# Kernel tuning notes

Measured on AMD Instinct MI355X. Metric: run time of the kernel, lower is better.

The kernel has to match this reference:

```python
import jax, jax.numpy as jnp
import numpy as np

N, E, F_IN, G = 100000, 1600000, 128, 64
H1, H2, H3 = 64, 32, 16


def _xavier(key, fan_in, fan_out):
    lim = np.sqrt(6.0 / (fan_in + fan_out))
    return jax.random.uniform(key, (fan_in, fan_out), jnp.float32, -lim, lim)


def setup_inputs() -> dict:
    key = jax.random.key(0)
    ks = jax.random.split(key, 16)
    x = jax.random.normal(ks[0], (N, F_IN), jnp.float32)
    edge_index = jax.random.randint(ks[1], (2, E), 0, N, dtype=jnp.int32)
    batch = jnp.sort(jax.random.randint(ks[2], (N,), 0, G, dtype=jnp.int32))
    d = {
        "x": x,
        "W1": _xavier(ks[3], F_IN, H1), "b1": jnp.zeros((H1,), jnp.float32),
        "W2": _xavier(ks[4], H1, H2), "b2": jnp.zeros((H2,), jnp.float32),
        "W3": _xavier(ks[5], H2, H3), "b3": jnp.zeros((H3,), jnp.float32),
        "g1": jnp.ones((H1,), jnp.float32), "be1": jnp.zeros((H1,), jnp.float32),
        "g2": jnp.ones((H2,), jnp.float32), "be2": jnp.zeros((H2,), jnp.float32),
        "g3": jnp.ones((H3,), jnp.float32), "be3": jnp.zeros((H3,), jnp.float32),
        "attn_w": _xavier(ks[6], 3 * H3, 3), "attn_b": jnp.zeros((3,), jnp.float32),
        "fc1_w": _xavier(ks[7], H3, H3), "fc1_b": jnp.zeros((H3,), jnp.float32),
        "fc2_w": _xavier(ks[8], H3, H3 // 2), "fc2_b": jnp.zeros((H3 // 2,), jnp.float32),
        "out_w": _xavier(ks[9], H3 // 2, 1), "out_b": jnp.zeros((1,), jnp.float32),
        "edge_index": edge_index,
        "batch": batch,
        "num_graphs": G,
    }
    return d


def _lrelu(z):
    return jnp.where(z > 0, z, 0.1 * z)


def _bn(h, gamma, beta, eps=1e-5):
    # BatchNorm1d forward with batch statistics (biased variance), as torch training-mode math
    m = jnp.mean(h, axis=0)
    v = jnp.mean(jnp.square(h - m), axis=0)
    return (h - m) * jax.lax.rsqrt(v + eps) * gamma + beta


def reference(x, W1, b1, W2, b2, W3, b3, g1, be1, g2, be2, g3, be3,
              attn_w, attn_b, fc1_w, fc1_b, fc2_w, fc2_b, out_w, out_b,
              edge_index, batch, num_graphs):
    src, dst = edge_index[0], edge_index[1]
    n = x.shape[0]
    # GCN degree with self-loops: deg[i] = 1 + #incoming edges
    deg = jax.ops.segment_sum(jnp.ones((src.shape[0],), x.dtype), dst, num_segments=n) + 1.0
    dis = jax.lax.rsqrt(deg)                      # deg^-1/2, [N]
    enorm = dis[src] * dis[dst]                   # per-edge norm, [E]
    selfw = dis * dis                             # self-loop norm, [N]

    def gcn(h, W, b):
        hw = h @ W                                # [N, H]
        agg = jax.ops.segment_sum(hw[src] * enorm[:, None], dst, num_segments=n)
        return agg + selfw[:, None] * hw + b

    x1 = _lrelu(_bn(gcn(x, W1, b1), g1, be1))     # dropout = identity (eval)
    x2 = _lrelu(_bn(gcn(x1, W2, b2), g2, be2))    # residual skipped: 64 != 32
    x3 = _lrelu(_bn(gcn(x2, W3, b3), g3, be3))    # residual skipped: 32 != 16

    # multi-pool over graphs
    ones_n = jnp.ones((n,), x.dtype)
    counts = jax.ops.segment_sum(ones_n, batch, num_segments=num_graphs)  # [G]
    x_sum = jax.ops.segment_sum(x3, batch, num_segments=num_graphs)       # [G, H3]
    x_mean = x_sum / jnp.maximum(counts, 1.0)[:, None]
    x_max = jax.ops.segment_max(x3, batch, num_segments=num_graphs)

    pooled = jnp.concatenate([x_mean, x_max, x_sum], axis=1)              # [G, 3*H3]
    aw = jax.nn.softmax(pooled @ attn_w + attn_b, axis=1)                 # [G, 3]
    xg = aw[:, 0:1] * x_mean + aw[:, 1:2] * x_max + aw[:, 2:3] * x_sum    # [G, H3]

    xg = _lrelu(xg @ fc1_w + fc1_b)
    xg = _lrelu(xg @ fc2_w + fc2_b)
    out = jax.nn.sigmoid(xg @ out_w + out_b)                              # [G, 1]
    return out
```

## Files before the change

kernel.cpp:

```cpp
#include <hip/hip_runtime.h>

#define GG 64
typedef unsigned long long ull;
typedef unsigned short u16;

__device__ __forceinline__ u16 f2b(float x) {
    unsigned u = __float_as_uint(x);
    return (u16)((u + 0x7FFFu + ((u >> 16) & 1u)) >> 16);
}

__device__ __forceinline__ void add8(const uint4 q, float* acc) {
    acc[0] += __uint_as_float(q.x << 16);
    acc[1] += __uint_as_float(q.x & 0xFFFF0000u);
    acc[2] += __uint_as_float(q.y << 16);
    acc[3] += __uint_as_float(q.y & 0xFFFF0000u);
    acc[4] += __uint_as_float(q.z << 16);
    acc[5] += __uint_as_float(q.z & 0xFFFF0000u);
    acc[6] += __uint_as_float(q.w << 16);
    acc[7] += __uint_as_float(q.w & 0xFFFF0000u);
}

__global__ void k_hist(const int* __restrict__ dst, int* __restrict__ cnt, int E) {
    int e = blockIdx.x * blockDim.x + threadIdx.x;
    if (e < E) atomicAdd(&cnt[dst[e]], 1);
}

__global__ void k_dis(const int* __restrict__ cnt, float* __restrict__ dis, int n) {
    int i = blockIdx.x * blockDim.x + threadIdx.x;
    if (i < n) dis[i] = rsqrtf((float)cnt[i] + 1.0f);
}

__global__ void k_scanA(const int* __restrict__ cnt, int* __restrict__ rp,
                        int* __restrict__ bsum, int n) {
    __shared__ int s[256];
    int i = blockIdx.x * 256 + threadIdx.x;
    int v = (i < n) ? cnt[i] : 0;
    s[threadIdx.x] = v;
    __syncthreads();
    for (int off = 1; off < 256; off <<= 1) {
        int t = (threadIdx.x >= off) ? s[threadIdx.x - off] : 0;
        __syncthreads();
        s[threadIdx.x] += t;
        __syncthreads();
    }
    if (i < n) rp[i] = s[threadIdx.x] - v;
    if (threadIdx.x == 255) bsum[blockIdx.x] = s[255];
}

__global__ void k_scanB(int* __restrict__ bsum, int nb) {
    __shared__ int s[512];
    int v = (threadIdx.x < nb) ? bsum[threadIdx.x] : 0;
    s[threadIdx.x] = v;
    __syncthreads();
    for (int off = 1; off < 512; off <<= 1) {
        int t = (threadIdx.x >= off) ? s[threadIdx.x - off] : 0;
        __syncthreads();
        s[threadIdx.x] += t;
        __syncthreads();
    }
    if (threadIdx.x < nb) bsum[threadIdx.x] = s[threadIdx.x] - v;
}

__global__ void k_scanC(int* __restrict__ rp, const int* __restrict__ bsum,
                        int* __restrict__ cursor, int n, int E) {
    int i = blockIdx.x * 256 + threadIdx.x;
    if (i < n) {
        int r = rp[i] + bsum[blockIdx.x];
        rp[i] = r;
        cursor[i] = r;
    }
    if (i == 0) rp[n] = E;
}

__global__ __launch_bounds__(256) void k_scatter(const int* __restrict__ src,
                                                 const int* __restrict__ dst,
                                                 int* __restrict__ cursor,
                                                 ull* __restrict__ epack, int E, int n) {
    const int part = blockIdx.x & 7;
    const int nblk = gridDim.x >> 3;
    const int bser = blockIdx.x >> 3;
    const int lo = (int)(((long long)part * n) >> 3);
    const int hi = (part == 7) ? n : (int)(((long long)(part + 1) * n) >> 3);
    for (int e = bser * 256 + threadIdx.x; e < E; e += nblk * 256) {
        int d = dst[e];
        if (d >= lo && d < hi) {
            int s = src[e];
            int pos = atomicAdd(&cursor[d], 1);
            epack[pos] = (ull)(unsigned)s;
        }
    }
}

template <int FIN, int FOUT, bool BN>
__global__ __launch_bounds__(256) void k_mm(const float* __restrict__ h,
                                            const float* __restrict__ W,
                                            const float* __restrict__ dis,
                                            const float* __restrict__ stats,
                                            const float* __restrict__ gma,
                                            const float* __restrict__ bta,
                                            u16* __restrict__ hw, int n) {
    constexpr int FX  = FOUT / 4;
    constexpr int TY  = 256 / FX;
    constexpr int NT  = TY * 4;
    constexpr int LDA = FIN + ((FOUT == 64) ? 2 : 1);
    __shared__ float sA[NT * LDA];
    __shared__ float sW[FIN * FOUT];
    __shared__ float sSc[FIN], sSh[FIN];

    if (BN && threadIdx.x < FIN) {
        int f = threadIdx.x;
        float inv_n = 1.0f / (float)n;
        float m = stats[f] * inv_n;
        float var = fmaxf(stats[64 + f] * inv_n - m * m, 0.f);
        float sc = rsqrtf(var + 1e-5f) * gma[f];
        sSc[f] = sc;
        sSh[f] = bta[f] - m * sc;
    }
    for (int i = threadIdx.x; i < FIN * FOUT / 4; i += 256)
        ((float4*)sW)[i] = ((const float4*)W)[i];
    if (BN) __syncthreads();

    const int node0 = blockIdx.x * NT;
    constexpr int LD4 = NT * FIN / 4 / 256;
    #pragma unroll
    for (int i = 0; i < LD4; ++i) {
        int idx4 = i * 256 + threadIdx.x;
        int row = idx4 / (FIN / 4);
        int c4  = idx4 % (FIN / 4);
        int gn  = node0 + row;
        float4 v = make_float4(0.f, 0.f, 0.f, 0.f);
        if (gn < n) v = ((const float4*)(h + (long long)gn * FIN))[c4];
        if (BN) {
            int f = c4 * 4;
            float t;
            t = fmaf(v.x, sSc[f + 0], sSh[f + 0]); v.x = t > 0.f ? t : 0.1f * t;
            t = fmaf(v.y, sSc[f + 1], sSh[f + 1]); v.y = t > 0.f ? t : 0.1f * t;
            t = fmaf(v.z, sSc[f + 2], sSh[f + 2]); v.z = t > 0.f ? t : 0.1f * t;
            t = fmaf(v.w, sSc[f + 3], sSh[f + 3]); v.w = t > 0.f ? t : 0.1f * t;
        }
        float* p = &sA[row * LDA + c4 * 4];
        p[0] = v.x; p[1] = v.y; p[2] = v.z; p[3] = v.w;
    }
    __syncthreads();

    const int tx = threadIdx.x % FX;
    const int ty = threadIdx.x / FX;
    float acc[4][4];
    #pragma unroll
    for (int i = 0; i < 4; ++i)
        #pragma unroll
        for (int j = 0; j < 4; ++j) acc[i][j] = 0.f;

    #pragma unroll 8
    for (int k = 0; k < FIN; ++k) {
        float4 wv = *((const float4*)&sW[k * FOUT + tx * 4]);
        float a0 = sA[(ty * 4 + 0) * LDA + k];
        float a1 = sA[(ty * 4 + 1) * LDA + k];
        float a2 = sA[(ty * 4 + 2) * LDA + k];
        float a3 = sA[(ty * 4 + 3) * LDA + k];
        acc[0][0] = fmaf(a0, wv.x, acc[0][0]); acc[0][1] = fmaf(a0, wv.y, acc[0][1]);
        acc[0][2] = fmaf(a0, wv.z, acc[0][2]); acc[0][3] = fmaf(a0, wv.w, acc[0][3]);
        acc[1][0] = fmaf(a1, wv.x, acc[1][0]); acc[1][1] = fmaf(a1, wv.y, acc[1][1]);
        acc[1][2] = fmaf(a1, wv.z, acc[1][2]); acc[1][3] = fmaf(a1, wv.w, acc[1][3]);
        acc[2][0] = fmaf(a2, wv.x, acc[2][0]); acc[2][1] = fmaf(a2, wv.y, acc[2][1]);
        acc[2][2] = fmaf(a2, wv.z, acc[2][2]); acc[2][3] = fmaf(a2, wv.w, acc[2][3]);
        acc[3][0] = fmaf(a3, wv.x, acc[3][0]); acc[3][1] = fmaf(a3, wv.y, acc[3][1]);
        acc[3][2] = fmaf(a3, wv.z, acc[3][2]); acc[3][3] = fmaf(a3, wv.w, acc[3][3]);
    }

    #pragma unroll
    for (int i = 0; i < 4; ++i) {
        int gn = node0 + ty * 4 + i;
        if (gn < n) {
            float dv = dis[gn];
            ushort4 o;
            o.x = f2b(acc[i][0] * dv); o.y = f2b(acc[i][1] * dv);
            o.z = f2b(acc[i][2] * dv); o.w = f2b(acc[i][3] * dv);
            ((ushort4*)(hw + (long long)gn * FOUT))[tx] = o;
        }
    }
}

template <int FOUT>
__global__ __launch_bounds__(256) void k_agg(const u16* __restrict__ hwb,
                                             const ull* __restrict__ epack,
                                             const int* __restrict__ rp,
                                             const float* __restrict__ dis,
                                             const float* __restrict__ bias,
                                             float* __restrict__ y,
                                             float* __restrict__ stats, int n) {
    constexpr int LPN = FOUT / 8;
    constexpr int NPB = 256 / LPN;
    constexpr int RS  = FOUT / 8;
    __shared__ float ssum[FOUT], ssq[FOUT];
    for (int i = threadIdx.x; i < FOUT; i += 256) { ssum[i] = 0.f; ssq[i] = 0.f; }
    __syncthreads();
    const int local = threadIdx.x / LPN;
    const int fq = threadIdx.x % LPN;
    const uint4* hw4 = (const uint4*)hwb;
    float b8[8];
    #pragma unroll
    for (int i = 0; i < 8; ++i) b8[i] = bias[fq * 8 + i];
    float lsum[8] = {0,0,0,0,0,0,0,0}, lsq[8] = {0,0,0,0,0,0,0,0};

    int node = blockIdx.x * NPB + local;
    if (node < n) {
        int j0 = rp[node], j1 = rp[node + 1];
        float acc[8] = {0,0,0,0,0,0,0,0};
        int j = j0;
        for (; j + 8 <= j1; j += 8) {
            int s0 = (int)(unsigned)epack[j + 0];
            int s1 = (int)(unsigned)epack[j + 1];
            int s2 = (int)(unsigned)epack[j + 2];
            int s3 = (int)(unsigned)epack[j + 3];
            int s4 = (int)(unsigned)epack[j + 4];
            int s5 = (int)(unsigned)epack[j + 5];
            int s6 = (int)(unsigned)epack[j + 6];
            int s7 = (int)(unsigned)epack[j + 7];
            uint4 q0 = hw4[(long long)s0 * RS + fq];
            uint4 q1 = hw4[(long long)s1 * RS + fq];
            uint4 q2 = hw4[(long long)s2 * RS + fq];
            uint4 q3 = hw4[(long long)s3 * RS + fq];
            uint4 q4 = hw4[(long long)s4 * RS + fq];
            uint4 q5 = hw4[(long long)s5 * RS + fq];
            uint4 q6 = hw4[(long long)s6 * RS + fq];
            uint4 q7 = hw4[(long long)s7 * RS + fq];
            add8(q0, acc); add8(q1, acc); add8(q2, acc); add8(q3, acc);
            add8(q4, acc); add8(q5, acc); add8(q6, acc); add8(q7, acc);
        }
        for (; j + 2 <= j1; j += 2) {
            int s0 = (int)(unsigned)epack[j + 0];
            int s1 = (int)(unsigned)epack[j + 1];
            uint4 q0 = hw4[(long long)s0 * RS + fq];
            uint4 q1 = hw4[(long long)s1 * RS + fq];
            add8(q0, acc); add8(q1, acc);
        }
        for (; j < j1; ++j) {
            uint4 q = hw4[(long long)(unsigned)epack[j] * RS + fq];
            add8(q, acc);
        }
        uint4 qs = hw4[(long long)node * RS + fq];
        add8(qs, acc);
        float dv = dis[node];
        #pragma unroll
        for (int i = 0; i < 8; ++i) acc[i] = fmaf(dv, acc[i], b8[i]);
        float4* y4 = (float4*)y;
        long long o = (long long)node * (FOUT / 4) + fq * 2;
        y4[o]     = make_float4(acc[0], acc[1], acc[2], acc[3]);
        y4[o + 1] = make_float4(acc[4], acc[5], acc[6], acc[7]);
        #pragma unroll
        for (int i = 0; i < 8; ++i) {
            lsum[i] += acc[i];
            lsq[i] = fmaf(acc[i], acc[i], lsq[i]);
        }
    }
    #pragma unroll
    for (int i = 0; i < 8; ++i) {
        atomicAdd(&ssum[fq * 8 + i], lsum[i]);
        atomicAdd(&ssq[fq * 8 + i], lsq[i]);
    }
    __syncthreads();
    for (int i = threadIdx.x; i < FOUT; i += 256) {
        atomicAdd(&stats[i], ssum[i]);
        atomicAdd(&stats[64 + i], ssq[i]);
    }
}

__global__ void k_pool_graph(const float* __restrict__ yraw, const int* __restrict__ batch,
                             const float* __restrict__ stats, const float* __restrict__ gma,
                             const float* __restrict__ bta, int n,
                             float* __restrict__ psum, float* __restrict__ pmax,
                             float* __restrict__ pcnt) {
    const int g = blockIdx.x;
    const int f = threadIdx.x & 15;
    float inv_n = 1.0f / (float)n;
    float m = stats[f] * inv_n;
    float var = fmaxf(stats[64 + f] * inv_n - m * m, 0.f);
    float sc = rsqrtf(var + 1e-5f) * gma[f];
    float sh = bta[f] - m * sc;

    __shared__ int s_lo, s_hi;
    if (threadIdx.x == 0) {
        int lo = 0, hi = n;
        while (lo < hi) { int mid = (lo + hi) >> 1; if (batch[mid] < g) lo = mid + 1; else hi = mid; }
        s_lo = lo;
        hi = n;
        while (lo < hi) { int mid = (lo + hi) >> 1; if (batch[mid] < g + 1) lo = mid + 1; else hi = mid; }
        s_hi = lo;
    }
    __syncthreads();
    const int start = s_lo, end = s_hi;
    float lsum = 0.f, lmax = -3.0e38f;
    for (long long idx = (long long)start * 16 + threadIdx.x; idx < (long long)end * 16; idx += blockDim.x) {
        float t = fmaf(yraw[idx], sc, sh);
        float v = t > 0.f ? t : 0.1f * t;
        lsum += v;
        lmax = fmaxf(lmax, v);
    }
    __shared__ float ss[256], sm[256];
    ss[threadIdx.x] = lsum; sm[threadIdx.x] = lmax;
    __syncthreads();
    for (int off = 128; off >= 16; off >>= 1) {
        if (threadIdx.x < off) {
            ss[threadIdx.x] += ss[threadIdx.x + off];
            sm[threadIdx.x] = fmaxf(sm[threadIdx.x], sm[threadIdx.x + off]);
        }
        __syncthreads();
    }
    if (threadIdx.x < 16) {
        psum[g * 16 + threadIdx.x] = ss[threadIdx.x];
        pmax[g * 16 + threadIdx.x] = sm[threadIdx.x];
    }
    if (threadIdx.x == 0) pcnt[g] = (float)(end - start);
}

__global__ void k_head(const float* __restrict__ psum, const float* __restrict__ pmax,
                       const float* __restrict__ pcnt,
                       const float* __restrict__ attn_w, const float* __restrict__ attn_b,
                       const float* __restrict__ fc1_w, const float* __restrict__ fc1_b,
                       const float* __restrict__ fc2_w, const float* __restrict__ fc2_b,
                       const float* __restrict__ out_w, const float* __restrict__ out_b,
                       float* __restrict__ out) {
    int g = threadIdx.x;
    if (g >= GG) return;
    float xs[16], xm[16], xx[16];
    float c = fmaxf(pcnt[g], 1.0f);
    for (int f = 0; f < 16; ++f) {
        xs[f] = psum[(g << 4) + f];
        xm[f] = xs[f] / c;
        xx[f] = pmax[(g << 4) + f];
    }
    float lg[3];
    for (int cI = 0; cI < 3; ++cI) {
        float a = attn_b[cI];
        for (int f = 0; f < 16; ++f) {
            a += xm[f] * attn_w[f * 3 + cI];
            a += xx[f] * attn_w[(16 + f) * 3 + cI];
            a += xs[f] * attn_w[(32 + f) * 3 + cI];
        }
        lg[cI] = a;
    }
    float mx = fmaxf(lg[0], fmaxf(lg[1], lg[2]));
    float e0 = expf(lg[0] - mx), e1 = expf(lg[1] - mx), e2 = expf(lg[2] - mx);
    float inv = 1.0f / (e0 + e1 + e2);
    float a0 = e0 * inv, a1 = e1 * inv, a2 = e2 * inv;
    float xg[16];
    for (int f = 0; f < 16; ++f) xg[f] = a0 * xm[f] + a1 * xx[f] + a2 * xs[f];
    float t1[16];
    for (int j = 0; j < 16; ++j) {
        float a = fc1_b[j];
        for (int k = 0; k < 16; ++k) a += xg[k] * fc1_w[k * 16 + j];
        t1[j] = a > 0.f ? a : 0.1f * a;
    }
    float t2[8];
    for (int j = 0; j < 8; ++j) {
        float a = fc2_b[j];
        for (int k = 0; k < 16; ++k) a += t1[k] * fc2_w[k * 8 + j];
        t2[j] = a > 0.f ? a : 0.1f * a;
    }
    float o = out_b[0];
    for (int k = 0; k < 8; ++k) o += t2[k] * out_w[k];
    o = 1.0f / (1.0f + expf(-o));
    out[g] = o;
}

extern "C" void kernel_launch(void* const* d_in, const int* in_sizes, int n_in,
                              void* d_out, int out_size, void* d_ws, size_t ws_size,
                              hipStream_t stream) {
    const float* x      = (const float*)d_in[0];
    const float* W1     = (const float*)d_in[1];  const float* b1   = (const float*)d_in[2];
    const float* W2     = (const float*)d_in[3];  const float* b2   = (const float*)d_in[4];
    const float* W3     = (const float*)d_in[5];  const float* b3   = (const float*)d_in[6];
    const float* g1     = (const float*)d_in[7];  const float* be1  = (const float*)d_in[8];
    const float* g2     = (const float*)d_in[9];  const float* be2  = (const float*)d_in[10];
    const float* g3     = (const float*)d_in[11]; const float* be3  = (const float*)d_in[12];
    const float* attn_w = (const float*)d_in[13]; const float* attn_b = (const float*)d_in[14];
    const float* fc1_w  = (const float*)d_in[15]; const float* fc1_b  = (const float*)d_in[16];
    const float* fc2_w  = (const float*)d_in[17]; const float* fc2_b  = (const float*)d_in[18];
    const float* out_w  = (const float*)d_in[19]; const float* out_b  = (const float*)d_in[20];
    const int* edge_index = (const int*)d_in[21];
    const int* batch      = (const int*)d_in[22];

    const int N = in_sizes[0] / 128;
    const int E = in_sizes[21] / 2;
    const int* srcp = edge_index;
    const int* dstp = edge_index + E;
    const int nb = (N + 255) / 256;

    char* ws = (char*)d_ws;
    float* dis    = (float*)(ws);
    int*   cnt    = (int*)(ws + 0x80000);
    int*   rp     = (int*)(ws + 0x100000);
    int*   bsum   = (int*)(ws + 0x180000);
    float* stats1 = (float*)(ws + 0x182000);
    float* stats2 = stats1 + 128;
    float* stats3 = stats2 + 128;
    float* psum   = stats3 + 128;
    float* pmax   = psum + GG * 16;
    float* pcnt   = pmax + GG * 16;
    ull*   epack  = (ull*)(ws + 0x190000);
    float* buf1   = (float*)(ws + 0x190000 + (size_t)E * 8);
    u16*   hwb    = (u16*)(buf1 + (size_t)N * 64);

    hipMemsetAsync(cnt, 0, (size_t)N * 4, stream);
    k_hist<<<(E + 255) / 256, 256, 0, stream>>>(dstp, cnt, E);
    k_dis<<<nb, 256, 0, stream>>>(cnt, dis, N);
    k_scanA<<<nb, 256, 0, stream>>>(cnt, rp, bsum, N);
    k_scanB<<<1, 512, 0, stream>>>(bsum, nb);
    k_scanC<<<nb, 256, 0, stream>>>(rp, bsum, cnt, N, E);
    k_scatter<<<2048, 256, 0, stream>>>(srcp, dstp, cnt, epack, E, N);
    hipMemsetAsync(stats1, 0, 3 * 512, stream);

    const int gr1 = (N + 31) / 32;
    const int gr2 = (N + 63) / 64;
    const int gr3 = (N + 127) / 128;

    k_mm<128, 64, false><<<(N + 63) / 64, 256, 0, stream>>>(
        x, W1, dis, nullptr, nullptr, nullptr, hwb, N);
    k_agg<64><<<gr1, 256, 0, stream>>>(hwb, epack, rp, dis, b1, buf1, stats1, N);

    k_mm<64, 32, true><<<(N + 127) / 128, 256, 0, stream>>>(
        buf1, W2, dis, stats1, g1, be1, hwb, N);
    k_agg<32><<<gr2, 256, 0, stream>>>(hwb, epack, rp, dis, b2, buf1, stats2, N);

    k_mm<32, 16, true><<<(N + 255) / 256, 256, 0, stream>>>(
        buf1, W3, dis, stats2, g2, be2, hwb, N);
    k_agg<16><<<gr3, 256, 0, stream>>>(hwb, epack, rp, dis, b3, buf1, stats3, N);

    k_pool_graph<<<GG, 256, 0, stream>>>(buf1, batch, stats3, g3, be3, N, psum, pmax, pcnt);
    k_head<<<1, 64, 0, stream>>>(psum, pmax, pcnt, attn_w, attn_b,
                                 fc1_w, fc1_b, fc2_w, fc2_b, out_w, out_b,
                                 (float*)d_out);
}
```

Measured before the change: 588.8 us.

## Shrink edge list to int32, partition histogram, fuse dis into scan, persist agg

Stores the CSR source indices as 32-bit ints instead of 64-bit, halving edge-list traffic in scatter and all three aggregation passes. The histogram kernel now uses the same 8-way destination-range partitioning as scatter, meant to localise atomics per XCD. The rsqrt degree computation is folded into the first scan kernel, removing a launch. Aggregation kernels use a fixed 2048-block grid-stride loop, which amortises per-block stat reductions but may reduce latency hiding if occupancy drops.

```diff
diff --git a/kernel.cpp b/kernel.cpp
--- a/kernel.cpp
+++ b/kernel.cpp
@@ -20,21 +20,25 @@
     acc[7] += __uint_as_float(q.w & 0xFFFF0000u);
 }
 
-__global__ void k_hist(const int* __restrict__ dst, int* __restrict__ cnt, int E) {
-    int e = blockIdx.x * blockDim.x + threadIdx.x;
-    if (e < E) atomicAdd(&cnt[dst[e]], 1);
-}
-
-__global__ void k_dis(const int* __restrict__ cnt, float* __restrict__ dis, int n) {
-    int i = blockIdx.x * blockDim.x + threadIdx.x;
-    if (i < n) dis[i] = rsqrtf((float)cnt[i] + 1.0f);
+__global__ __launch_bounds__(256) void k_hist(const int* __restrict__ dst,
+                                              int* __restrict__ cnt, int E, int n) {
+    const int part = blockIdx.x & 7;
+    const int nblk = gridDim.x >> 3;
+    const int bser = blockIdx.x >> 3;
+    const int lo = (int)(((long long)part * n) >> 3);
+    const int hi = (part == 7) ? n : (int)(((long long)(part + 1) * n) >> 3);
+    for (int e = bser * 256 + threadIdx.x; e < E; e += nblk * 256) {
+        int d = dst[e];
+        if (d >= lo && d < hi) atomicAdd(&cnt[d], 1);
+    }
 }
 
 __global__ void k_scanA(const int* __restrict__ cnt, int* __restrict__ rp,
-                        int* __restrict__ bsum, int n) {
+                        int* __restrict__ bsum, float* __restrict__ dis, int n) {
     __shared__ int s[256];
     int i = blockIdx.x * 256 + threadIdx.x;
     int v = (i < n) ? cnt[i] : 0;
+    if (i < n) dis[i] = rsqrtf((float)v + 1.0f);
     s[threadIdx.x] = v;
     __syncthreads();
     for (int off = 1; off < 256; off <<= 1) {
@@ -75,7 +79,7 @@
 __global__ __launch_bounds__(256) void k_scatter(const int* __restrict__ src,
                                                  const int* __restrict__ dst,
                                                  int* __restrict__ cursor,
-                                                 ull* __restrict__ epack, int E, int n) {
+                                                 int* __restrict__ epack, int E, int n) {
     const int part = blockIdx.x & 7;
     const int nblk = gridDim.x >> 3;
     const int bser = blockIdx.x >> 3;
@@ -86,7 +90,7 @@
         if (d >= lo && d < hi) {
             int s = src[e];
             int pos = atomicAdd(&cursor[d], 1);
-            epack[pos] = (ull)(unsigned)s;
+            epack[pos] = s;
         }
     }
 }
@@ -183,7 +187,7 @@
 
 template <int FOUT>
 __global__ __launch_bounds__(256) void k_agg(const u16* __restrict__ hwb,
-                                             const ull* __restrict__ epack,
+                                             const int* __restrict__ epack,
                                              const int* __restrict__ rp,
                                              const float* __restrict__ dis,
                                              const float* __restrict__ bias,
@@ -203,20 +207,18 @@
     for (int i = 0; i < 8; ++i) b8[i] = bias[fq * 8 + i];
     float lsum[8] = {0,0,0,0,0,0,0,0}, lsq[8] = {0,0,0,0,0,0,0,0};
 
-    int node = blockIdx.x * NPB + local;
-    if (node < n) {
+    for (long long base = (long long)blockIdx.x * NPB; base < n;
+         base += (long long)gridDim.x * NPB) {
+        int node = (int)base + local;
+        if (node >= n) continue;
         int j0 = rp[node], j1 = rp[node + 1];
         float acc[8] = {0,0,0,0,0,0,0,0};
         int j = j0;
         for (; j + 8 <= j1; j += 8) {
-            int s0 = (int)(unsigned)epack[j + 0];
-            int s1 = (int)(unsigned)epack[j + 1];
-            int s2 = (int)(unsigned)epack[j + 2];
-            int s3 = (int)(unsigned)epack[j + 3];
-            int s4 = (int)(unsigned)epack[j + 4];
-            int s5 = (int)(unsigned)epack[j + 5];
-            int s6 = (int)(unsigned)epack[j + 6];
-            int s7 = (int)(unsigned)epack[j + 7];
+            int s0 = epack[j + 0], s1 = epack[j + 1];
+            int s2 = epack[j + 2], s3 = epack[j + 3];
+            int s4 = epack[j + 4], s5 = epack[j + 5];
+            int s6 = epack[j + 6], s7 = epack[j + 7];
             uint4 q0 = hw4[(long long)s0 * RS + fq];
             uint4 q1 = hw4[(long long)s1 * RS + fq];
             uint4 q2 = hw4[(long long)s2 * RS + fq];
@@ -229,14 +231,13 @@
             add8(q4, acc); add8(q5, acc); add8(q6, acc); add8(q7, acc);
         }
         for (; j + 2 <= j1; j += 2) {
-            int s0 = (int)(unsigned)epack[j + 0];
-            int s1 = (int)(unsigned)epack[j + 1];
+            int s0 = epack[j + 0], s1 = epack[j + 1];
             uint4 q0 = hw4[(long long)s0 * RS + fq];
             uint4 q1 = hw4[(long long)s1 * RS + fq];
             add8(q0, acc); add8(q1, acc);
         }
         for (; j < j1; ++j) {
-            uint4 q = hw4[(long long)(unsigned)epack[j] * RS + fq];
+            uint4 q = hw4[(long long)epack[j] * RS + fq];
             add8(q, acc);
         }
         uint4 qs = hw4[(long long)node * RS + fq];
@@ -398,34 +399,29 @@
     float* psum   = stats3 + 128;
     float* pmax   = psum + GG * 16;
     float* pcnt   = pmax + GG * 16;
-    ull*   epack  = (ull*)(ws + 0x190000);
-    float* buf1   = (float*)(ws + 0x190000 + (size_t)E * 8);
+    int*   epack  = (int*)(ws + 0x190000);
+    float* buf1   = (float*)(ws + 0x190000 + (size_t)E * 4);
     u16*   hwb    = (u16*)(buf1 + (size_t)N * 64);
 
     hipMemsetAsync(cnt, 0, (size_t)N * 4, stream);
-    k_hist<<<(E + 255) / 256, 256, 0, stream>>>(dstp, cnt, E);
-    k_dis<<<nb, 256, 0, stream>>>(cnt, dis, N);
-    k_scanA<<<nb, 256, 0, stream>>>(cnt, rp, bsum, N);
+    k_hist<<<2048, 256, 0, stream>>>(dstp, cnt, E, N);
+    k_scanA<<<nb, 256, 0, stream>>>(cnt, rp, bsum, dis, N);
     k_scanB<<<1, 512, 0, stream>>>(bsum, nb);
     k_scanC<<<nb, 256, 0, stream>>>(rp, bsum, cnt, N, E);
     k_scatter<<<2048, 256, 0, stream>>>(srcp, dstp, cnt, epack, E, N);
     hipMemsetAsync(stats1, 0, 3 * 512, stream);
 
-    const int gr1 = (N + 31) / 32;
-    const int gr2 = (N + 63) / 64;
-    const int gr3 = (N + 127) / 128;
-
     k_mm<128, 64, false><<<(N + 63) / 64, 256, 0, stream>>>(
         x, W1, dis, nullptr, nullptr, nullptr, hwb, N);
-    k_agg<64><<<gr1, 256, 0, stream>>>(hwb, epack, rp, dis, b1, buf1, stats1, N);
+    k_agg<64><<<2048, 256, 0, stream>>>(hwb, epack, rp, dis, b1, buf1, stats1, N);
 
     k_mm<64, 32, true><<<(N + 127) / 128, 256, 0, stream>>>(
         buf1, W2, dis, stats1, g1, be1, hwb, N);
-    k_agg<32><<<gr2, 256, 0, stream>>>(hwb, epack, rp, dis, b2, buf1, stats2, N);
+    k_agg<32><<<2048, 256, 0, stream>>>(hwb, epack, rp, dis, b2, buf1, stats2, N);
 
     k_mm<32, 16, true><<<(N + 255) / 256, 256, 0, stream>>>(
         buf1, W3, dis, stats2, g2, be2, hwb, N);
-    k_agg<16><<<gr3, 256, 0, stream>>>(hwb, epack, rp, dis, b3, buf1, stats3, N);
+    k_agg<16><<<2048, 256, 0, stream>>>(hwb, epack, rp, dis, b3, buf1, stats3, N);
 
     k_pool_graph<<<GG, 256, 0, stream>>>(buf1, batch, stats3, g3, be3, N, psum, pmax, pcnt);
     k_head<<<1, 64, 0, stream>>>(psum, pmax, pcnt, attn_w, attn_b,
```

After: 599.3 us. No clear change (+1.8%).
